# Performance work log

Measured on AMD Instinct MI355X. Metric: run time of the kernel, lower is better.

## Reference

```python
import jax, jax.numpy as jnp
import numpy as np

B, D_IN, H1, H2, A = 8192, 512, 4096, 4096, 64
QMIN, QMAX = -128.0, 127.0  # int8 saturation range


def _int_vals(key, shape, spread):
    # integer-valued fixed-point tensor stored as float32
    return jnp.clip(jnp.round(jax.random.normal(key, shape) * spread), QMIN * spread, QMAX * spread).astype(jnp.float32)


def setup_inputs() -> dict:
    key = jax.random.key(0)
    ks = jax.random.split(key, 9)
    x = jnp.clip(jnp.round(jax.random.normal(ks[0], (B, D_IN)) * 32.0), QMIN, QMAX).astype(jnp.float32)
    w1 = jnp.clip(jnp.round(jax.random.normal(ks[1], (H1, D_IN)) * 16.0), QMIN, QMAX).astype(jnp.float32)
    b1 = _int_vals(ks[2], (H1,), 256.0)
    w2 = jnp.clip(jnp.round(jax.random.normal(ks[3], (H2, H1)) * 16.0), QMIN, QMAX).astype(jnp.float32)
    b2 = _int_vals(ks[4], (H2,), 256.0)
    w_mu = jnp.clip(jnp.round(jax.random.normal(ks[5], (A, H2)) * 16.0), QMIN, QMAX).astype(jnp.float32)
    b_mu = _int_vals(ks[6], (A,), 256.0)
    w_prob = jnp.clip(jnp.round(jax.random.normal(ks[7], (A, H2)) * 16.0), QMIN, QMAX).astype(jnp.float32)
    b_prob = _int_vals(ks[8], (A,), 256.0)
    M = jnp.full((1,), 2.0 ** -10, dtype=jnp.float32)  # per-layer requant multiplier
    s = jnp.full((1,), 0.05, dtype=jnp.float32)        # activation quantize scale
    return {
        "x": x, "w1": w1, "b1": b1, "w2": w2, "b2": b2,
        "w_mu": w_mu, "b_mu": b_mu, "w_prob": w_prob, "b_prob": b_prob,
        "M1": M, "M2": M, "M_mu": M, "M_prob": M,
        "s2": s, "s_mu": s, "s_prob": s,
    }


def _qlinear(x, w, b, M):
    # genesys fixed-point linear: int accumulate then requantize by multiplier M
    acc = jnp.matmul(x, w.T) + b  # integer-valued fp32 accumulator
    return jnp.round(M * acc)


def _quantize(src, scale, zero_point=0.0):
    return jnp.clip(jnp.round(src / scale) + zero_point, QMIN, QMAX)


def reference(x, w1, b1, w2, b2, w_mu, b_mu, w_prob, b_prob, M1, M2, M_mu, M_prob, s2, s_mu, s_prob):
    h = jax.nn.relu(_qlinear(x, w1, b1, M1))
    h = _quantize(h, s2)
    h = jax.nn.relu(_qlinear(h, w2, b2, M2))
    # NOTE: original forward_int feeds the un-quantized relu output into the
    # heads (x_mu/x_prob quantizations are dead code) and returns only prob.
    prob = _qlinear(h, w_prob, b_prob, M_prob)
    return prob
```

## Files before the change

### kernel.cpp

```cpp
#include <hip/hip_runtime.h>
#include <stdint.h>

#define NB   8192
#define DIN  512
#define NH1  4096
#define NH2  4096
#define NA   64

typedef int v4i __attribute__((ext_vector_type(4)));

__device__ __forceinline__ void gload16(const void* g, const void* l) {
    __builtin_amdgcn_global_load_lds(
        (const __attribute__((address_space(1))) void*)(uintptr_t)g,
        (__attribute__((address_space(3))) void*)(uint32_t)(uintptr_t)l,
        16, 0, 0);
}

__global__ void cvt_i8(const float* __restrict__ in, signed char* __restrict__ out, int n4) {
    const int i = blockIdx.x * blockDim.x + threadIdx.x;
    if (i >= n4) return;
    const float4 v = ((const float4*)in)[i];
    char4 c;
    c.x = (signed char)__float2int_rn(v.x);
    c.y = (signed char)__float2int_rn(v.y);
    c.z = (signed char)__float2int_rn(v.z);
    c.w = (signed char)__float2int_rn(v.w);
    ((char4*)out)[i] = c;
}

__global__ void sum_wp(const float* __restrict__ wp, int* __restrict__ S) {
    __shared__ int red[256];
    const int a = blockIdx.x, t = threadIdx.x;
    int p = 0;
    for (int k = t; k < NH2; k += 256) p += __float2int_rn(wp[(size_t)a * NH2 + k]);
    red[t] = p; __syncthreads();
    for (int s = 128; s > 0; s >>= 1) { if (t < s) red[t] += red[t + s]; __syncthreads(); }
    if (t == 0) S[a] = red[0];
}

template <int EPI>
__global__ __launch_bounds__(512, 4)
void gemm_i8_t3(const signed char* __restrict__ Ag,
                const signed char* __restrict__ Bg,
                int M, int N, int K,
                const float* __restrict__ bias,
                const float* __restrict__ Mscale,
                const float* __restrict__ qscale,
                signed char* __restrict__ out0,
                signed char* __restrict__ out1)
{
    __shared__ __align__(16) signed char lds[3][24576];

    const int tid  = threadIdx.x;
    const int lane = tid & 63;
    const int wid  = tid >> 6;
    const int wm   = wid >> 1, wn = wid & 1;

    const int nwg  = gridDim.x;
    const int bid  = blockIdx.x;
    const int swzb = (bid & 7) * (nwg >> 3) + (bid >> 3);
    const int nbx  = N >> 7;
    const int bx   = swzb % nbx;
    const int by   = swzb / nbx;
    const int bm0  = by << 8, bn0 = bx << 7;

    const int srow  = tid >> 2;
    const int sclog = (tid & 3) ^ ((tid >> 3) & 3);
    const signed char* aS = Ag + (size_t)(bm0 + srow) * K + sclog * 16;
    const signed char* bS = Bg + (size_t)(bn0 + srow) * K + sclog * 16;
    const size_t rK = (size_t)128 * K;

    #define STAGE(bp, ko) do { \
        gload16(aS + (ko),      &lds[bp][0]     + tid * 16); \
        gload16(aS + rK + (ko), &lds[bp][8192]  + tid * 16); \
        gload16(bS + (ko),      &lds[bp][16384] + tid * 16); } while (0)

    const int r    = lane & 15;
    const int pc   = ((lane >> 4) ^ ((r >> 1) & 3)) * 16;
    const int aoff = wm * 4096 + r * 64 + pc;
    const int boff = 16384 + wn * 4096 + r * 64 + pc;

    const int nt = K >> 6;

    STAGE(0, 0);
    STAGE(1, 64);

    v4i acc[4][4] = {};
    int cur = 0, nxt = 2;

    for (int t = 0; t < nt; ++t) {
        if (t < nt - 1) asm volatile("s_waitcnt vmcnt(3)" ::: "memory");
        else            asm volatile("s_waitcnt vmcnt(0)" ::: "memory");
        __builtin_amdgcn_s_barrier();

        const signed char* L = &lds[cur][0];
        v4i af[4], bf[4];
        #pragma unroll
        for (int m = 0; m < 4; ++m) af[m] = *(const v4i*)(L + aoff + m * 1024);
        #pragma unroll
        for (int n = 0; n < 4; ++n) bf[n] = *(const v4i*)(L + boff + n * 1024);

        if (t + 2 < nt) STAGE(nxt, (t + 2) << 6);

        __builtin_amdgcn_s_setprio(1);
        #pragma unroll
        for (int m = 0; m < 4; ++m)
            #pragma unroll
            for (int n = 0; n < 4; ++n)
                acc[m][n] = __builtin_amdgcn_mfma_i32_16x16x64_i8(af[m], bf[n], acc[m][n], 0, 0, 0);
        __builtin_amdgcn_s_setprio(0);
        __builtin_amdgcn_s_barrier();

        cur = (cur == 2) ? 0 : cur + 1;
        nxt = (nxt == 2) ? 0 : nxt + 1;
    }
    #undef STAGE

    const int rowb = wm * 64 + ((lane >> 4) << 2);
    const int colb = wn * 64 + (lane & 15);
    signed char* img0 = (signed char*)&lds[0][0];
    signed char* img1 = img0 + 34816;

    if constexpr (EPI == 1) {
        const float Mv = Mscale[0];
        const float sv = qscale[0];
        #pragma unroll
        for (int n = 0; n < 4; ++n) {
            const int col  = colb + n * 16;
            const int bint = __float2int_rn(bias[bn0 + col]);
            #pragma unroll
            for (int m = 0; m < 4; ++m) {
                #pragma unroll
                for (int j = 0; j < 4; ++j) {
                    const int row  = rowb + m * 16 + j;
                    const int accv = acc[m][n][j] + bint;
                    float h = rintf(Mv * (float)accv);
                    h = fmaxf(h, 0.0f);
                    float q = rintf(h / sv);
                    q = fminf(fmaxf(q, -128.0f), 127.0f);
                    img0[row * 136 + col] = (signed char)(int)q;
                }
            }
        }
        __syncthreads();
        #pragma unroll
        for (int p = 0; p < 8; ++p) {
            const int idx = p * 512 + tid;
            const int row = idx >> 4;
            const int cb  = (idx & 15) * 8;
            *(int2*)(out0 + (size_t)(bm0 + row) * N + bn0 + cb) =
                *(const int2*)(img0 + row * 136 + cb);
        }
    } else {
        const float Mv = Mscale[0];
        #pragma unroll
        for (int n = 0; n < 4; ++n) {
            const int col  = colb + n * 16;
            const int bint = __float2int_rn(bias[bn0 + col]);
            #pragma unroll
            for (int m = 0; m < 4; ++m) {
                #pragma unroll
                for (int j = 0; j < 4; ++j) {
                    const int row  = rowb + m * 16 + j;
                    const int accv = acc[m][n][j] + bint;
                    double rr = rint((double)Mv * (double)accv);
                    rr = rr > 0.0 ? rr : 0.0;
                    const int v = (int)rr;
                    img0[row * 136 + col] = (signed char)((v & 255) - 128);
                    img1[row * 136 + col] = (signed char)((v >> 8) - 128);
                }
            }
        }
        __syncthreads();
        #pragma unroll
        for (int p = 0; p < 8; ++p) {
            const int idx = p * 512 + tid;
            const int row = idx >> 4;
            const int cb  = (idx & 15) * 8;
            const size_t g = (size_t)(bm0 + row) * N + bn0 + cb;
            *(int2*)(out0 + g) = *(const int2*)(img0 + row * 136 + cb);
            *(int2*)(out1 + g) = *(const int2*)(img1 + row * 136 + cb);
        }
    }
}

__global__ __launch_bounds__(512, 1)
void head_mfma(const signed char* __restrict__ lo,
               const signed char* __restrict__ hi,
               const signed char* __restrict__ wpq,
               int* __restrict__ part)
{
    __shared__ __align__(16) signed char Bl[32768];
    __shared__ __align__(16) signed char Al[3][32768];

    const int tid  = threadIdx.x;
    const int lane = tid & 63;
    const int wid  = tid >> 6;
    const int rblk = blockIdx.x >> 3;
    const int kblk = blockIdx.x & 7;
    const int bm0  = rblk << 8;
    const int kb   = kblk << 9;

    #pragma unroll
    for (int s = 0; s < 4; ++s) {
        const int brow = s * 16 + (tid >> 5);
        const int pch  = tid & 31;
        const int lc   = pch ^ (brow & 7);
        gload16(wpq + (size_t)brow * NH2 + kb + lc * 16, Bl + brow * 512 + pch * 16);
    }

    const int srow  = tid >> 2;
    const int sclog = (tid & 3) ^ ((tid >> 3) & 3);
    const size_t ab = (size_t)(bm0 + srow) * NH2 + kb + sclog * 16;
    const size_t rK = (size_t)128 * NH2;

    #define HSTAGE(bp, ko) do { \
        gload16(lo + ab + (ko),      &Al[bp][0]     + tid * 16); \
        gload16(lo + ab + rK + (ko), &Al[bp][8192]  + tid * 16); \
        gload16(hi + ab + (ko),      &Al[bp][16384] + tid * 16); \
        gload16(hi + ab + rK + (ko), &Al[bp][24576] + tid * 16); } while (0)

    HSTAGE(0, 0);
    HSTAGE(1, 64);

    const int r    = lane & 15;
    const int cg   = lane >> 4;
    const int pcA  = (cg ^ ((r >> 1) & 3)) * 16;
    const int aoff = wid * 2048 + r * 64 + pcA;

    v4i accL[2][4] = {}, accH[2][4] = {};
    int cur = 0, nxt = 2;

    for (int t = 0; t < 8; ++t) {
        if (t < 7) asm volatile("s_waitcnt vmcnt(4)" ::: "memory");
        else       asm volatile("s_waitcnt vmcnt(0)" ::: "memory");
        __builtin_amdgcn_s_barrier();

        const signed char* A = &Al[cur][0];
        v4i bf[4], al[2], ah[2];
        #pragma unroll
        for (int n = 0; n < 4; ++n)
            bf[n] = *(const v4i*)(Bl + (n * 16 + r) * 512 + (((t * 4 + cg) ^ (r & 7)) * 16));
        #pragma unroll
        for (int m = 0; m < 2; ++m) al[m] = *(const v4i*)(A + aoff + m * 1024);
        #pragma unroll
        for (int m = 0; m < 2; ++m) ah[m] = *(const v4i*)(A + 16384 + aoff + m * 1024);

        if (t + 2 < 8) HSTAGE(nxt, (t + 2) << 6);

        __builtin_amdgcn_s_setprio(1);
        #pragma unroll
        for (int m = 0; m < 2; ++m)
            #pragma unroll
            for (int n = 0; n < 4; ++n) {
                accL[m][n] = __builtin_amdgcn_mfma_i32_16x16x64_i8(al[m], bf[n], accL[m][n], 0, 0, 0);
                accH[m][n] = __builtin_amdgcn_mfma_i32_16x16x64_i8(ah[m], bf[n], accH[m][n], 0, 0, 0);
            }
        __builtin_amdgcn_s_setprio(0);
        __builtin_amdgcn_s_barrier();

        cur = (cur == 2) ? 0 : cur + 1;
        nxt = (nxt == 2) ? 0 : nxt + 1;
    }
    #undef HSTAGE

    int* pb = part + (size_t)kblk * (NB * NA);
    const int rowb = bm0 + wid * 32 + ((lane >> 4) << 2);
    #pragma unroll
    for (int m = 0; m < 2; ++m)
        #pragma unroll
        for (int n = 0; n < 4; ++n) {
            const int a = n * 16 + (lane & 15);
            #pragma unroll
            for (int j = 0; j < 4; ++j) {
                const int row = rowb + m * 16 + j;
                pb[(size_t)row * NA + a] = accL[m][n][j] + (accH[m][n][j] << 8);
            }
        }
}

__global__ __launch_bounds__(256)
void comb_head(const int* __restrict__ part, const int* __restrict__ S,
               const float* __restrict__ bp, const float* __restrict__ Mp,
               float* __restrict__ out)
{
    const int t = blockIdx.x * 256 + threadIdx.x;
    const int a = t & 63;
    long long sum = 0;
    #pragma unroll
    for (int c = 0; c < 8; ++c) sum += part[(size_t)c * (NB * NA) + t];
    sum += 32896LL * (long long)S[a] + (long long)__float2int_rn(bp[a]);
    out[t] = (float)rint((double)Mp[0] * (double)sum);
}

extern "C" void kernel_launch(void* const* d_in, const int* in_sizes, int n_in,
                              void* d_out, int out_size, void* d_ws, size_t ws_size,
                              hipStream_t stream) {
    const float* x  = (const float*)d_in[0];
    const float* w1 = (const float*)d_in[1];
    const float* b1 = (const float*)d_in[2];
    const float* w2 = (const float*)d_in[3];
    const float* b2 = (const float*)d_in[4];
    const float* wp = (const float*)d_in[7];
    const float* bp = (const float*)d_in[8];
    const float* M1 = (const float*)d_in[9];
    const float* M2 = (const float*)d_in[10];
    const float* Mp = (const float*)d_in[12];
    const float* s2 = (const float*)d_in[13];

    const size_t MB = (size_t)1 << 20;
    char* ws = (char*)d_ws;
    signed char* x_i8  = (signed char*)(ws);
    signed char* w1_i8 = (signed char*)(ws + 4  * MB);
    signed char* w2_i8 = (signed char*)(ws + 6  * MB);
    signed char* wp_i8 = (signed char*)(ws + 22 * MB);
    int*         Ssum  = (int*)        (ws + 22 * MB + 512 * 1024);
    signed char* h1q   = (signed char*)(ws + 23 * MB);
    signed char* h2lo  = (signed char*)(ws + 55 * MB);
    signed char* h2hi  = (signed char*)(ws + 87 * MB);
    int*         part  = (int*)        (ws);

    cvt_i8<<<dim3(4096),  dim3(256), 0, stream>>>(x,  x_i8,  NB  * DIN / 4);
    cvt_i8<<<dim3(2048),  dim3(256), 0, stream>>>(w1, w1_i8, NH1 * DIN / 4);
    cvt_i8<<<dim3(16384), dim3(256), 0, stream>>>(w2, w2_i8, NH2 * NH1 / 4);
    cvt_i8<<<dim3(256),   dim3(256), 0, stream>>>(wp, wp_i8, NA  * NH2 / 4);
    sum_wp<<<dim3(64), dim3(256), 0, stream>>>(wp, Ssum);

    gemm_i8_t3<1><<<dim3((NB / 256) * (NH1 / 128)), dim3(512), 0, stream>>>(
        x_i8, w1_i8, NB, NH1, DIN, b1, M1, s2, h1q, nullptr);
    gemm_i8_t3<2><<<dim3((NB / 256) * (NH2 / 128)), dim3(512), 0, stream>>>(
        h1q, w2_i8, NB, NH2, NH1, b2, M2, nullptr, h2lo, h2hi);
    head_mfma<<<dim3(256), dim3(512), 0, stream>>>(h2lo, h2hi, wp_i8, part);
    comb_head<<<dim3(NB * NA / 256), dim3(256), 0, stream>>>(part, Ssum, bp, Mp, (float*)d_out);
}
```

Measured before the change: 227.4 us.

## Rewrite int8 GEMM as 256x256 tile with 8-phase interleaved load/MFMA schedule

The main int8 GEMM kernel moves from a 256x128 tile with a 3-stage, 64-wide K pipeline to a 256x256 tile with a 128-wide K step. It double-buffers 64KB LDS stages and interleaves the global-to-LDS loads with four MFMA phases per K-step, using a 2x4 wave layout. The goal is more MFMA work per byte loaded and less global traffic per output, with better overlap of loads and compute. In exchange, occupancy drops to 2 workgroups, register pressure rises with 32 accumulators, and the h2 epilogue is serialized into two passes through one LDS image.

```diff
diff --git a/kernel.cpp b/kernel.cpp
--- a/kernel.cpp
+++ b/kernel.cpp
@@ -8,6 +8,10 @@
 #define NA   64
 
 typedef int v4i __attribute__((ext_vector_type(4)));
+
+__device__ __forceinline__ v4i mfma_i8(v4i a, v4i b, v4i c) {
+    return __builtin_amdgcn_mfma_i32_16x16x64_i8(a, b, c, 0, 0, 0);
+}
 
 __device__ __forceinline__ void gload16(const void* g, const void* l) {
     __builtin_amdgcn_global_load_lds(
@@ -39,149 +43,167 @@
 }
 
 template <int EPI>
-__global__ __launch_bounds__(512, 4)
-void gemm_i8_t3(const signed char* __restrict__ Ag,
-                const signed char* __restrict__ Bg,
-                int M, int N, int K,
-                const float* __restrict__ bias,
-                const float* __restrict__ Mscale,
-                const float* __restrict__ qscale,
-                signed char* __restrict__ out0,
-                signed char* __restrict__ out1)
+__global__ __launch_bounds__(512, 2)
+void gemm_8ph(const signed char* __restrict__ Ag,
+              const signed char* __restrict__ Bg,
+              int M, int N, int K,
+              const float* __restrict__ bias,
+              const float* __restrict__ Mscale,
+              const float* __restrict__ qscale,
+              signed char* __restrict__ out0,
+              signed char* __restrict__ out1)
 {
-    __shared__ __align__(16) signed char lds[3][24576];
+    __shared__ __align__(16) signed char lds[2][65536];
 
     const int tid  = threadIdx.x;
     const int lane = tid & 63;
     const int wid  = tid >> 6;
-    const int wm   = wid >> 1, wn = wid & 1;
+    const int wm   = wid >> 2, wn = wid & 3;
 
     const int nwg  = gridDim.x;
     const int bid  = blockIdx.x;
     const int swzb = (bid & 7) * (nwg >> 3) + (bid >> 3);
-    const int nbx  = N >> 7;
+    const int nbx  = N >> 8;
     const int bx   = swzb % nbx;
     const int by   = swzb / nbx;
-    const int bm0  = by << 8, bn0 = bx << 7;
-
-    const int srow  = tid >> 2;
-    const int sclog = (tid & 3) ^ ((tid >> 3) & 3);
-    const signed char* aS = Ag + (size_t)(bm0 + srow) * K + sclog * 16;
-    const signed char* bS = Bg + (size_t)(bn0 + srow) * K + sclog * 16;
-    const size_t rK = (size_t)128 * K;
-
-    #define STAGE(bp, ko) do { \
-        gload16(aS + (ko),      &lds[bp][0]     + tid * 16); \
-        gload16(aS + rK + (ko), &lds[bp][8192]  + tid * 16); \
-        gload16(bS + (ko),      &lds[bp][16384] + tid * 16); } while (0)
-
-    const int r    = lane & 15;
-    const int pc   = ((lane >> 4) ^ ((r >> 1) & 3)) * 16;
-    const int aoff = wm * 4096 + r * 64 + pc;
-    const int boff = 16384 + wn * 4096 + r * 64 + pc;
-
-    const int nt = K >> 6;
-
-    STAGE(0, 0);
-    STAGE(1, 64);
-
-    v4i acc[4][4] = {};
-    int cur = 0, nxt = 2;
-
-    for (int t = 0; t < nt; ++t) {
-        if (t < nt - 1) asm volatile("s_waitcnt vmcnt(3)" ::: "memory");
-        else            asm volatile("s_waitcnt vmcnt(0)" ::: "memory");
-        __builtin_amdgcn_s_barrier();
-
-        const signed char* L = &lds[cur][0];
-        v4i af[4], bf[4];
-        #pragma unroll
-        for (int m = 0; m < 4; ++m) af[m] = *(const v4i*)(L + aoff + m * 1024);
-        #pragma unroll
-        for (int n = 0; n < 4; ++n) bf[n] = *(const v4i*)(L + boff + n * 1024);
-
-        if (t + 2 < nt) STAGE(nxt, (t + 2) << 6);
-
-        __builtin_amdgcn_s_setprio(1);
-        #pragma unroll
-        for (int m = 0; m < 4; ++m)
-            #pragma unroll
-            for (int n = 0; n < 4; ++n)
-                acc[m][n] = __builtin_amdgcn_mfma_i32_16x16x64_i8(af[m], bf[n], acc[m][n], 0, 0, 0);
-        __builtin_amdgcn_s_setprio(0);
-        __builtin_amdgcn_s_barrier();
-
-        cur = (cur == 2) ? 0 : cur + 1;
-        nxt = (nxt == 2) ? 0 : nxt + 1;
+    const int bm0  = by << 8, bn0 = bx << 8;
+
+    const int srow = tid >> 2;
+    const int sc   = (((tid & 3) ^ ((tid >> 3) & 3)) << 4);
+    const signed char* aS = Ag + (size_t)(bm0 + srow) * K + sc;
+    const signed char* bS = Bg + (size_t)(bn0 + srow) * K + sc;
+    const size_t hK = (size_t)128 * K;
+    const int NTm = (K >> 7) - 1;
+
+#define STG(b, isB, h, t) do { \
+    const signed char* s_ = ((isB) ? bS : aS) + (size_t)(h) * hK + (size_t)((t) & NTm) * 128; \
+    signed char* d_ = &lds[b][0] + (isB) * 32768 + (h) * 16384 + tid * 16; \
+    gload16(s_,      d_); \
+    gload16(s_ + 64, d_ + 8192); } while (0)
+
+    const int rp = (lane & 15) * 64 + ((((lane >> 4) ^ ((lane >> 1) & 3)) & 3) << 4);
+    const int aB = wm * 4096 + rp;
+    const int bB = 32768 + wn * 1024 + rp;
+
+    STG(0, 0, 0, 0); STG(0, 0, 1, 0); STG(0, 1, 0, 0); STG(0, 1, 1, 0);
+    STG(1, 0, 0, 1); STG(1, 1, 0, 1); STG(1, 1, 1, 1);
+    asm volatile("s_waitcnt vmcnt(6)" ::: "memory");
+    asm volatile("s_barrier" ::: "memory");
+
+    v4i acc[8][4] = {};
+
+#define PHASE(mp, STG_STMT, WAIT_STMT) do { \
+    v4i a00 = *(const v4i*)(L + ((2*(mp)) >> 2) * 16384 +        ((2*(mp)) & 3) * 1024 + aB); \
+    v4i a01 = *(const v4i*)(L + ((2*(mp)) >> 2) * 16384 + 8192 + ((2*(mp)) & 3) * 1024 + aB); \
+    v4i a10 = *(const v4i*)(L + ((2*(mp)+1) >> 2) * 16384 +        ((2*(mp)+1) & 3) * 1024 + aB); \
+    v4i a11 = *(const v4i*)(L + ((2*(mp)+1) >> 2) * 16384 + 8192 + ((2*(mp)+1) & 3) * 1024 + aB); \
+    STG_STMT; \
+    WAIT_STMT; \
+    asm volatile("s_barrier" ::: "memory"); \
+    __builtin_amdgcn_s_setprio(1); \
+    _Pragma("unroll") \
+    for (int n = 0; n < 4; ++n) { \
+        acc[2*(mp)][n]   = mfma_i8(a00, bf[n][0], acc[2*(mp)][n]); \
+        acc[2*(mp)+1][n] = mfma_i8(a10, bf[n][0], acc[2*(mp)+1][n]); \
+    } \
+    _Pragma("unroll") \
+    for (int n = 0; n < 4; ++n) { \
+        acc[2*(mp)][n]   = mfma_i8(a01, bf[n][1], acc[2*(mp)][n]); \
+        acc[2*(mp)+1][n] = mfma_i8(a11, bf[n][1], acc[2*(mp)+1][n]); \
+    } \
+    __builtin_amdgcn_s_setprio(0); \
+    asm volatile("s_barrier" ::: "memory"); \
+} while (0)
+
+#define KSTEP(BUF, OBUF, TN) do { \
+    const signed char* L = &lds[BUF][0]; \
+    v4i bf[4][2]; \
+    _Pragma("unroll") \
+    for (int n = 0; n < 4; ++n) { \
+        bf[n][0] = *(const v4i*)(L + (n >> 1) * 16384 +        (n & 1) * 4096 + bB); \
+        bf[n][1] = *(const v4i*)(L + (n >> 1) * 16384 + 8192 + (n & 1) * 4096 + bB); \
+    } \
+    PHASE(0, STG(OBUF, 0, 1, TN),     (void)0); \
+    PHASE(1, STG(BUF,  1, 0, (TN)+1), (void)0); \
+    PHASE(2, STG(BUF,  1, 1, (TN)+1), (void)0); \
+    PHASE(3, STG(BUF,  0, 0, (TN)+1), asm volatile("s_waitcnt vmcnt(6)" ::: "memory")); \
+} while (0)
+
+    const int NI = (K >> 7) >> 1;
+    for (int i = 0; i < NI; ++i) {
+        const int t0 = 2 * i;
+        KSTEP(0, 1, t0 + 1);
+        KSTEP(1, 0, t0 + 2);
     }
-    #undef STAGE
-
-    const int rowb = wm * 64 + ((lane >> 4) << 2);
-    const int colb = wn * 64 + (lane & 15);
-    signed char* img0 = (signed char*)&lds[0][0];
-    signed char* img1 = img0 + 34816;
+#undef KSTEP
+#undef PHASE
+#undef STG
+
+    asm volatile("s_waitcnt vmcnt(0)" ::: "memory");
+    __syncthreads();
+    signed char* img = (signed char*)&lds[0][0];
+    const int fr = (lane >> 4) << 2;
+    const int fc = lane & 15;
+
+#define FLUSH(dst) do { \
+    _Pragma("unroll") \
+    for (int p = 0; p < 8; ++p) { \
+        const int idx = p * 512 + tid; \
+        const int row = idx >> 4, ch = (idx & 15) << 4; \
+        *(int4*)((dst) + (size_t)(bm0 + row) * N + bn0 + ch) = *(const int4*)(img + row * 264 + ch); \
+    } } while (0)
 
     if constexpr (EPI == 1) {
         const float Mv = Mscale[0];
         const float sv = qscale[0];
         #pragma unroll
         for (int n = 0; n < 4; ++n) {
-            const int col  = colb + n * 16;
-            const int bint = __float2int_rn(bias[bn0 + col]);
+            const int ecol = n * 64 + wn * 16 + fc;
+            const int bint = __float2int_rn(bias[bn0 + ecol]);
             #pragma unroll
-            for (int m = 0; m < 4; ++m) {
+            for (int m = 0; m < 8; ++m) {
+                const int erow = (m >> 2) * 128 + wm * 64 + (m & 3) * 16 + fr;
                 #pragma unroll
                 for (int j = 0; j < 4; ++j) {
-                    const int row  = rowb + m * 16 + j;
                     const int accv = acc[m][n][j] + bint;
                     float h = rintf(Mv * (float)accv);
                     h = fmaxf(h, 0.0f);
                     float q = rintf(h / sv);
                     q = fminf(fmaxf(q, -128.0f), 127.0f);
-                    img0[row * 136 + col] = (signed char)(int)q;
+                    img[(erow + j) * 264 + ecol] = (signed char)(int)q;
                 }
             }
         }
         __syncthreads();
-        #pragma unroll
-        for (int p = 0; p < 8; ++p) {
-            const int idx = p * 512 + tid;
-            const int row = idx >> 4;
-            const int cb  = (idx & 15) * 8;
-            *(int2*)(out0 + (size_t)(bm0 + row) * N + bn0 + cb) =
-                *(const int2*)(img0 + row * 136 + cb);
-        }
+        FLUSH(out0);
     } else {
         const float Mv = Mscale[0];
         #pragma unroll
-        for (int n = 0; n < 4; ++n) {
-            const int col  = colb + n * 16;
-            const int bint = __float2int_rn(bias[bn0 + col]);
+        for (int pass = 0; pass < 2; ++pass) {
             #pragma unroll
-            for (int m = 0; m < 4; ++m) {
+            for (int n = 0; n < 4; ++n) {
+                const int ecol = n * 64 + wn * 16 + fc;
+                const int bint = __float2int_rn(bias[bn0 + ecol]);
                 #pragma unroll
-                for (int j = 0; j < 4; ++j) {
-                    const int row  = rowb + m * 16 + j;
-                    const int accv = acc[m][n][j] + bint;
-                    double rr = rint((double)Mv * (double)accv);
-                    rr = rr > 0.0 ? rr : 0.0;
-                    const int v = (int)rr;
-                    img0[row * 136 + col] = (signed char)((v & 255) - 128);
-                    img1[row * 136 + col] = (signed char)((v >> 8) - 128);
+                for (int m = 0; m < 8; ++m) {
+                    const int erow = (m >> 2) * 128 + wm * 64 + (m & 3) * 16 + fr;
+                    #pragma unroll
+                    for (int j = 0; j < 4; ++j) {
+                        const int accv = acc[m][n][j] + bint;
+                        double rr = rint((double)Mv * (double)accv);
+                        rr = rr > 0.0 ? rr : 0.0;
+                        const int v = (int)rr;
+                        const int byte = pass ? ((v >> 8) - 128) : ((v & 255) - 128);
+                        img[(erow + j) * 264 + ecol] = (signed char)byte;
+                    }
                 }
             }
-        }
-        __syncthreads();
-        #pragma unroll
-        for (int p = 0; p < 8; ++p) {
-            const int idx = p * 512 + tid;
-            const int row = idx >> 4;
-            const int cb  = (idx & 15) * 8;
-            const size_t g = (size_t)(bm0 + row) * N + bn0 + cb;
-            *(int2*)(out0 + g) = *(const int2*)(img0 + row * 136 + cb);
-            *(int2*)(out1 + g) = *(const int2*)(img1 + row * 136 + cb);
+            __syncthreads();
+            if (pass == 0) { FLUSH(out0); __syncthreads(); }
+            else           { FLUSH(out1); }
         }
     }
+#undef FLUSH
 }
 
 __global__ __launch_bounds__(512, 1)
@@ -253,8 +275,8 @@
         for (int m = 0; m < 2; ++m)
             #pragma unroll
             for (int n = 0; n < 4; ++n) {
-                accL[m][n] = __builtin_amdgcn_mfma_i32_16x16x64_i8(al[m], bf[n], accL[m][n], 0, 0, 0);
-                accH[m][n] = __builtin_amdgcn_mfma_i32_16x16x64_i8(ah[m], bf[n], accH[m][n], 0, 0, 0);
+                accL[m][n] = mfma_i8(al[m], bf[n], accL[m][n]);
+                accH[m][n] = mfma_i8(ah[m], bf[n], accH[m][n]);
             }
         __builtin_amdgcn_s_setprio(0);
         __builtin_amdgcn_s_barrier();
@@ -326,9 +348,9 @@
     cvt_i8<<<dim3(256),   dim3(256), 0, stream>>>(wp, wp_i8, NA  * NH2 / 4);
     sum_wp<<<dim3(64), dim3(256), 0, stream>>>(wp, Ssum);
 
-    gemm_i8_t3<1><<<dim3((NB / 256) * (NH1 / 128)), dim3(512), 0, stream>>>(
+    gemm_8ph<1><<<dim3((NB / 256) * (NH1 / 256)), dim3(512), 0, stream>>>(
         x_i8, w1_i8, NB, NH1, DIN, b1, M1, s2, h1q, nullptr);
-    gemm_i8_t3<2><<<dim3((NB / 256) * (NH2 / 128)), dim3(512), 0, stream>>>(
+    gemm_8ph<2><<<dim3((NB / 256) * (NH2 / 256)), dim3(512), 0, stream>>>(
         h1q, w2_i8, NB, NH2, NH1, b2, M2, nullptr, h2lo, h2hi);
     head_mfma<<<dim3(256), dim3(512), 0, stream>>>(h2lo, h2hi, wp_i8, part);
     comb_head<<<dim3(NB * NA / 256), dim3(256), 0, stream>>>(part, Ssum, bp, Mp, (float*)d_out);
```

After: 221.9 us. -2.4%, faster.

## Shrink GEMM tile to 128x128 with 256 threads and double-buffered LDS

Applied to the files above, without the earlier changes.

Replaces the 256x128 tile, 512-thread, triple-buffered int8 GEMM with a 128x128 tile, 256-thread, double-buffered version. Grid order becomes M-major and the epilogue writes out in two passes through one smaller LDS image using 16-byte stores. The aim is lower LDS use and more concurrent workgroups per CU to raise occupancy. In exchange each tile loads more operand bytes per MFMA, and the pipeline prefetches only one stage ahead instead of two.

```diff
diff --git a/kernel.cpp b/kernel.cpp
--- a/kernel.cpp
+++ b/kernel.cpp
@@ -8,6 +8,10 @@
 #define NA   64
 
 typedef int v4i __attribute__((ext_vector_type(4)));
+
+__device__ __forceinline__ v4i mfma_i8(v4i a, v4i b, v4i c) {
+    return __builtin_amdgcn_mfma_i32_16x16x64_i8(a, b, c, 0, 0, 0);
+}
 
 __device__ __forceinline__ void gload16(const void* g, const void* l) {
     __builtin_amdgcn_global_load_lds(
@@ -39,17 +43,17 @@
 }
 
 template <int EPI>
-__global__ __launch_bounds__(512, 4)
-void gemm_i8_t3(const signed char* __restrict__ Ag,
-                const signed char* __restrict__ Bg,
-                int M, int N, int K,
-                const float* __restrict__ bias,
-                const float* __restrict__ Mscale,
-                const float* __restrict__ qscale,
-                signed char* __restrict__ out0,
-                signed char* __restrict__ out1)
+__global__ __launch_bounds__(256, 4)
+void gemm_sb(const signed char* __restrict__ Ag,
+             const signed char* __restrict__ Bg,
+             int M, int N, int K,
+             const float* __restrict__ bias,
+             const float* __restrict__ Mscale,
+             const float* __restrict__ qscale,
+             signed char* __restrict__ out0,
+             signed char* __restrict__ out1)
 {
-    __shared__ __align__(16) signed char lds[3][24576];
+    __shared__ __align__(16) signed char lds[2][16384];
 
     const int tid  = threadIdx.x;
     const int lane = tid & 63;
@@ -59,129 +63,124 @@
     const int nwg  = gridDim.x;
     const int bid  = blockIdx.x;
     const int swzb = (bid & 7) * (nwg >> 3) + (bid >> 3);
-    const int nbx  = N >> 7;
-    const int bx   = swzb % nbx;
-    const int by   = swzb / nbx;
-    const int bm0  = by << 8, bn0 = bx << 7;
-
-    const int srow  = tid >> 2;
-    const int sclog = (tid & 3) ^ ((tid >> 3) & 3);
-    const signed char* aS = Ag + (size_t)(bm0 + srow) * K + sclog * 16;
-    const signed char* bS = Bg + (size_t)(bn0 + srow) * K + sclog * 16;
-    const size_t rK = (size_t)128 * K;
-
-    #define STAGE(bp, ko) do { \
-        gload16(aS + (ko),      &lds[bp][0]     + tid * 16); \
-        gload16(aS + rK + (ko), &lds[bp][8192]  + tid * 16); \
-        gload16(bS + (ko),      &lds[bp][16384] + tid * 16); } while (0)
+    const int nby  = M >> 7;
+    const int by   = swzb % nby;
+    const int bx   = swzb / nby;
+    const int bm0  = by << 7, bn0 = bx << 7;
+
+    const int srow = tid >> 2;
+    const int sc   = (((tid & 3) ^ ((tid >> 3) & 3)) << 4);
+    const signed char* aS = Ag + (size_t)(bm0 + srow) * K + sc;
+    const signed char* bS = Bg + (size_t)(bn0 + srow) * K + sc;
+    const size_t hK = (size_t)64 * K;
+
+#define STG(bp, ko) do { \
+    gload16(aS + (ko),      &lds[bp][0]     + tid * 16); \
+    gload16(aS + hK + (ko), &lds[bp][4096]  + tid * 16); \
+    gload16(bS + (ko),      &lds[bp][8192]  + tid * 16); \
+    gload16(bS + hK + (ko), &lds[bp][12288] + tid * 16); } while (0)
 
     const int r    = lane & 15;
-    const int pc   = ((lane >> 4) ^ ((r >> 1) & 3)) * 16;
+    const int pc   = (((lane >> 4) ^ ((r >> 1) & 3)) << 4);
     const int aoff = wm * 4096 + r * 64 + pc;
-    const int boff = 16384 + wn * 4096 + r * 64 + pc;
+    const int boff = 8192 + wn * 4096 + r * 64 + pc;
 
     const int nt = K >> 6;
 
-    STAGE(0, 0);
-    STAGE(1, 64);
-
+    STG(0, 0);
     v4i acc[4][4] = {};
-    int cur = 0, nxt = 2;
 
     for (int t = 0; t < nt; ++t) {
-        if (t < nt - 1) asm volatile("s_waitcnt vmcnt(3)" ::: "memory");
-        else            asm volatile("s_waitcnt vmcnt(0)" ::: "memory");
+        if (t + 1 < nt) {
+            STG((t + 1) & 1, (t + 1) << 6);
+            asm volatile("s_waitcnt vmcnt(4)" ::: "memory");
+        } else {
+            asm volatile("s_waitcnt vmcnt(0)" ::: "memory");
+        }
         __builtin_amdgcn_s_barrier();
 
-        const signed char* L = &lds[cur][0];
+        const signed char* L = &lds[t & 1][0];
         v4i af[4], bf[4];
         #pragma unroll
         for (int m = 0; m < 4; ++m) af[m] = *(const v4i*)(L + aoff + m * 1024);
         #pragma unroll
         for (int n = 0; n < 4; ++n) bf[n] = *(const v4i*)(L + boff + n * 1024);
 
-        if (t + 2 < nt) STAGE(nxt, (t + 2) << 6);
-
         __builtin_amdgcn_s_setprio(1);
         #pragma unroll
         for (int m = 0; m < 4; ++m)
             #pragma unroll
             for (int n = 0; n < 4; ++n)
-                acc[m][n] = __builtin_amdgcn_mfma_i32_16x16x64_i8(af[m], bf[n], acc[m][n], 0, 0, 0);
+                acc[m][n] = mfma_i8(af[m], bf[n], acc[m][n]);
         __builtin_amdgcn_s_setprio(0);
         __builtin_amdgcn_s_barrier();
-
-        cur = (cur == 2) ? 0 : cur + 1;
-        nxt = (nxt == 2) ? 0 : nxt + 1;
     }
-    #undef STAGE
-
-    const int rowb = wm * 64 + ((lane >> 4) << 2);
-    const int colb = wn * 64 + (lane & 15);
-    signed char* img0 = (signed char*)&lds[0][0];
-    signed char* img1 = img0 + 34816;
+#undef STG
+
+    __syncthreads();
+    signed char* img = (signed char*)&lds[0][0];
+    const int fr = (lane >> 4) << 2;
+    const int fc = lane & 15;
+
+#define FLUSH(dst) do { \
+    _Pragma("unroll") \
+    for (int p = 0; p < 4; ++p) { \
+        const int idx = p * 256 + tid; \
+        const int row = idx >> 3, ch = (idx & 7) << 4; \
+        *(int4*)((dst) + (size_t)(bm0 + row) * N + bn0 + ch) = *(const int4*)(img + row * 144 + ch); \
+    } } while (0)
 
     if constexpr (EPI == 1) {
         const float Mv = Mscale[0];
         const float sv = qscale[0];
         #pragma unroll
         for (int n = 0; n < 4; ++n) {
-            const int col  = colb + n * 16;
-            const int bint = __float2int_rn(bias[bn0 + col]);
+            const int ecol = wn * 64 + n * 16 + fc;
+            const int bint = __float2int_rn(bias[bn0 + ecol]);
             #pragma unroll
             for (int m = 0; m < 4; ++m) {
+                const int erow = wm * 64 + m * 16 + fr;
                 #pragma unroll
                 for (int j = 0; j < 4; ++j) {
-                    const int row  = rowb + m * 16 + j;
                     const int accv = acc[m][n][j] + bint;
                     float h = rintf(Mv * (float)accv);
                     h = fmaxf(h, 0.0f);
                     float q = rintf(h / sv);
                     q = fminf(fmaxf(q, -128.0f), 127.0f);
-                    img0[row * 136 + col] = (signed char)(int)q;
+                    img[(erow + j) * 144 + ecol] = (signed char)(int)q;
                 }
             }
         }
         __syncthreads();
-        #pragma unroll
-        for (int p = 0; p < 8; ++p) {
-            const int idx = p * 512 + tid;
-            const int row = idx >> 4;
-            const int cb  = (idx & 15) * 8;
-            *(int2*)(out0 + (size_t)(bm0 + row) * N + bn0 + cb) =
-                *(const int2*)(img0 + row * 136 + cb);
-        }
+        FLUSH(out0);
     } else {
         const float Mv = Mscale[0];
         #pragma unroll
-        for (int n = 0; n < 4; ++n) {
-            const int col  = colb + n * 16;
-            const int bint = __float2int_rn(bias[bn0 + col]);
-            #pragma unroll
-            for (int m = 0; m < 4; ++m) {
+        for (int pass = 0; pass < 2; ++pass) {
+            #pragma unroll
+            for (int n = 0; n < 4; ++n) {
+                const int ecol = wn * 64 + n * 16 + fc;
+                const int bint = __float2int_rn(bias[bn0 + ecol]);
                 #pragma unroll
-                for (int j = 0; j < 4; ++j) {
-                    const int row  = rowb + m * 16 + j;
-                    const int accv = acc[m][n][j] + bint;
-                    double rr = rint((double)Mv * (double)accv);
-                    rr = rr > 0.0 ? rr : 0.0;
-                    const int v = (int)rr;
-                    img0[row * 136 + col] = (signed char)((v & 255) - 128);
-                    img1[row * 136 + col] = (signed char)((v >> 8) - 128);
+                for (int m = 0; m < 4; ++m) {
+                    const int erow = wm * 64 + m * 16 + fr;
+                    #pragma unroll
+                    for (int j = 0; j < 4; ++j) {
+                        const int accv = acc[m][n][j] + bint;
+                        double rr = rint((double)Mv * (double)accv);
+                        rr = rr > 0.0 ? rr : 0.0;
+                        const int v = (int)rr;
+                        const int byte = pass ? ((v >> 8) - 128) : ((v & 255) - 128);
+                        img[(erow + j) * 144 + ecol] = (signed char)byte;
+                    }
                 }
             }
-        }
-        __syncthreads();
-        #pragma unroll
-        for (int p = 0; p < 8; ++p) {
-            const int idx = p * 512 + tid;
-            const int row = idx >> 4;
-            const int cb  = (idx & 15) * 8;
-            const size_t g = (size_t)(bm0 + row) * N + bn0 + cb;
-            *(int2*)(out0 + g) = *(const int2*)(img0 + row * 136 + cb);
-            *(int2*)(out1 + g) = *(const int2*)(img1 + row * 136 + cb);
+            __syncthreads();
+            if (pass == 0) { FLUSH(out0); __syncthreads(); }
+            else           { FLUSH(out1); }
         }
     }
+#undef FLUSH
 }
 
 __global__ __launch_bounds__(512, 1)
@@ -253,8 +252,8 @@
         for (int m = 0; m < 2; ++m)
             #pragma unroll
             for (int n = 0; n < 4; ++n) {
-                accL[m][n] = __builtin_amdgcn_mfma_i32_16x16x64_i8(al[m], bf[n], accL[m][n], 0, 0, 0);
-                accH[m][n] = __builtin_amdgcn_mfma_i32_16x16x64_i8(ah[m], bf[n], accH[m][n], 0, 0, 0);
+                accL[m][n] = mfma_i8(al[m], bf[n], accL[m][n]);
+                accH[m][n] = mfma_i8(ah[m], bf[n], accH[m][n]);
             }
         __builtin_amdgcn_s_setprio(0);
         __builtin_amdgcn_s_barrier();
@@ -326,9 +325,9 @@
     cvt_i8<<<dim3(256),   dim3(256), 0, stream>>>(wp, wp_i8, NA  * NH2 / 4);
     sum_wp<<<dim3(64), dim3(256), 0, stream>>>(wp, Ssum);
 
-    gemm_i8_t3<1><<<dim3((NB / 256) * (NH1 / 128)), dim3(512), 0, stream>>>(
+    gemm_sb<1><<<dim3((NB / 128) * (NH1 / 128)), dim3(256), 0, stream>>>(
         x_i8, w1_i8, NB, NH1, DIN, b1, M1, s2, h1q, nullptr);
-    gemm_i8_t3<2><<<dim3((NB / 256) * (NH2 / 128)), dim3(512), 0, stream>>>(
+    gemm_sb<2><<<dim3((NB / 128) * (NH2 / 128)), dim3(256), 0, stream>>>(
         h1q, w2_i8, NB, NH2, NH1, b2, M2, nullptr, h2lo, h2hi);
     head_mfma<<<dim3(256), dim3(512), 0, stream>>>(h2lo, h2hi, wp_i8, part);
     comb_head<<<dim3(NB * NA / 256), dim3(256), 0, stream>>>(part, Ssum, bp, Mp, (float*)d_out);
```

New measurement: 256.2 us. +12.6%, slower.
